# Kernel tuning notes

Measured on AMD Instinct MI355X. Metric: run time of the kernel, lower is better.

Reference implementation:

```python
import jax, jax.numpy as jnp
import numpy as np
import math

N_EMBD = 1024
N_HEAD = 16
B, T = 4, 2048

def setup_inputs() -> dict:
    key = jax.random.key(0)
    k1, k2, k3, k4 = jax.random.split(key, 4)
    x = jax.random.normal(k1, (B, T, N_EMBD), dtype=jnp.float32)
    # torch Linear weights: [out, in]; init scale ~1/sqrt(in)
    s = 1.0 / math.sqrt(N_EMBD)
    W_attn = jax.random.normal(k2, (3 * N_EMBD, N_EMBD), dtype=jnp.float32) * s
    W_proj = jax.random.normal(k3, (N_EMBD, N_EMBD), dtype=jnp.float32) * s
    b_proj = jax.random.normal(k4, (N_EMBD,), dtype=jnp.float32) * s
    return {"x": x, "W_attn": W_attn, "W_proj": W_proj, "b_proj": b_proj}

def reference(x, W_attn, W_proj, b_proj):
    Bx, Tx, C = x.shape
    hd = C // N_HEAD
    qkv = jnp.einsum('btc,oc->bto', x, W_attn)  # [B,T,3C]
    q, k, v = jnp.split(qkv, 3, axis=2)
    # [B, H, T, hd]
    q = q.reshape(Bx, Tx, N_HEAD, hd).transpose(0, 2, 1, 3)
    k = k.reshape(Bx, Tx, N_HEAD, hd).transpose(0, 2, 1, 3)
    v = v.reshape(Bx, Tx, N_HEAD, hd).transpose(0, 2, 1, 3)
    # NOTE: source divides by (1/sqrt(hd)) => MULTIPLIES by sqrt(hd). Faithful.
    att = jnp.einsum('bhqd,bhkd->bhqk', q, k) * jnp.sqrt(jnp.float32(hd))
    causal = jnp.tril(jnp.ones((Tx, Tx), dtype=bool))
    att = jnp.where(causal[None, None, :, :], att, -jnp.inf)
    att = jax.nn.softmax(att, axis=-1)
    y = jnp.einsum('bhqk,bhkd->bhqd', att, v)
    y = y.transpose(0, 2, 1, 3).reshape(Bx, Tx, C)
    y = jnp.einsum('btc,oc->bto', y, W_proj) + b_proj
    return y  # dropout is identity in eval
```

## Files before the change

### kernel.cpp

```cpp
#include <hip/hip_runtime.h>
#include <math.h>

#define BATCH 4
#define TSEQ  2048
#define CEMB  1024
#define NHEAD 16
#define HD    64
#define MROWS (BATCH * TSEQ)
#define QSCALE 11.5415603271f

typedef _Float16 half8 __attribute__((ext_vector_type(8)));
typedef _Float16 half4 __attribute__((ext_vector_type(4)));
typedef float    floatx4 __attribute__((ext_vector_type(4)));

#define GLOBAL_AS __attribute__((address_space(1)))
#define LDS_AS    __attribute__((address_space(3)))

__device__ __forceinline__ void lds_dma16(const _Float16* g, _Float16* l) {
    __builtin_amdgcn_global_load_lds((const GLOBAL_AS unsigned int*)g,
                                     (LDS_AS unsigned int*)l, 16, 0, 0);
}

__device__ __forceinline__ float fast_exp2(float x) {
    float r; asm("v_exp_f32 %0, %1" : "=v"(r) : "v"(x)); return r;
}

__global__ __launch_bounds__(256)
void cvt_fp16(const float* __restrict__ x, const float* __restrict__ wa,
              const float* __restrict__ wp, _Float16* __restrict__ x16,
              _Float16* __restrict__ wa16, _Float16* __restrict__ wp16)
{
    const int n1 = (BATCH * TSEQ * CEMB) / 4;
    const int n2 = (3 * CEMB * CEMB) / 4;
    int i = blockIdx.x * 256 + threadIdx.x;
    const float* src; _Float16* dst; int j;
    if (i < n1)            { src = x;  dst = x16;  j = i; }
    else if (i < n1 + n2)  { src = wa; dst = wa16; j = i - n1; }
    else                   { src = wp; dst = wp16; j = i - n1 - n2; }
    float4 v = ((const float4*)src)[j];
    half4 h = { (_Float16)v.x, (_Float16)v.y, (_Float16)v.z, (_Float16)v.w };
    ((half4*)dst)[j] = h;
}

__device__ __forceinline__ void stage32(const _Float16* __restrict__ gbase,
                                        _Float16* __restrict__ lds,
                                        int row0, int kk, int tid)
{
#pragma unroll
    for (int p = 0; p < 2; ++p) {
        int ci  = p * 256 + tid;
        int row = ci >> 2, pcc = ci & 3;
        int c   = pcc ^ (row & 3);
        lds_dma16(gbase + (size_t)(row0 + row) * CEMB + kk + c * 8, lds + ci * 8);
    }
}

__global__ __launch_bounds__(256)
void qkv_gemm(const _Float16* __restrict__ A, const _Float16* __restrict__ B,
              _Float16* __restrict__ q16, _Float16* __restrict__ k16,
              _Float16* __restrict__ v16)
{
    __shared__ __align__(16) _Float16 smem[16384];
    const int tid = threadIdx.x, lane = tid & 63, wave = tid >> 6;
    const int wm = wave & 1, wn = wave >> 1;
    const int m0 = blockIdx.y * 128, n0 = blockIdx.x * 128;
    const int l15 = lane & 15, quad = lane >> 4;

    floatx4 acc[4][4];
#pragma unroll
    for (int i = 0; i < 4; ++i)
#pragma unroll
        for (int j = 0; j < 4; ++j) acc[i][j] = (floatx4){0.f, 0.f, 0.f, 0.f};

    stage32(A, smem, m0, 0, tid);
    stage32(B, smem + 8192, n0, 0, tid);
    for (int kt = 0; kt < 32; ++kt) {
        const int cur = kt & 1;
        _Float16* Asc = smem + cur * 4096;
        _Float16* Bsc = smem + 8192 + cur * 4096;
        __syncthreads();
        if (kt < 31) {
            stage32(A, smem + (cur ^ 1) * 4096, m0, (kt + 1) * 32, tid);
            stage32(B, smem + 8192 + (cur ^ 1) * 4096, n0, (kt + 1) * 32, tid);
        }
        half8 af[4], bf[4];
#pragma unroll
        for (int mt = 0; mt < 4; ++mt) {
            int row = wm * 64 + mt * 16 + l15;
            af[mt] = *(const half8*)(Asc + row * 32 + (quad ^ (row & 3)) * 8);
        }
#pragma unroll
        for (int nt = 0; nt < 4; ++nt) {
            int row = wn * 64 + nt * 16 + l15;
            bf[nt] = *(const half8*)(Bsc + row * 32 + (quad ^ (row & 3)) * 8);
        }
#pragma unroll
        for (int mt = 0; mt < 4; ++mt)
#pragma unroll
            for (int nt = 0; nt < 4; ++nt)
                acc[mt][nt] = __builtin_amdgcn_mfma_f32_16x16x32_f16(af[mt], bf[nt], acc[mt][nt], 0, 0, 0);
    }

    __syncthreads();
    const int rbase = quad << 2;
    if (n0 < 2 * CEMB) {
        const float scale = (n0 < CEMB) ? QSCALE : 1.0f;
#pragma unroll
        for (int mt = 0; mt < 4; ++mt)
#pragma unroll
            for (int nt = 0; nt < 4; ++nt)
#pragma unroll
                for (int r = 0; r < 4; ++r) {
                    int t = wm * 64 + mt * 16 + rbase + r;
                    int n = wn * 64 + nt * 16 + l15;
                    int pc = (n >> 3) ^ (t & 15);
                    smem[t * 128 + pc * 8 + (n & 7)] = (_Float16)(acc[mt][nt][r] * scale);
                }
        __syncthreads();
        const int chunk = tid & 7;
#pragma unroll
        for (int i = 0; i < 8; ++i) {
            int gr = (tid >> 3) + i * 32;
            int seg = gr >> 7, t = gr & 127;
            int pc = (seg * 8 + chunk) ^ (t & 15);
            half8 v = *(const half8*)(smem + t * 128 + pc * 8);
            int gm = m0 + t, b = gm >> 11, tt = gm & (TSEQ - 1);
            int gnb = n0 + seg * 64;
            _Float16* dst;
            if (n0 < CEMB) {
                int h = gnb >> 6;
                dst = q16 + (((size_t)(b * NHEAD + h)) * TSEQ + tt) * HD;
            } else {
                int h = (gnb - CEMB) >> 6;
                dst = k16 + (((size_t)(b * NHEAD + h)) * TSEQ + tt) * HD;
            }
            *(half8*)(dst + chunk * 8) = v;
        }
    } else {
#pragma unroll
        for (int mt = 0; mt < 4; ++mt)
#pragma unroll
            for (int nt = 0; nt < 4; ++nt)
#pragma unroll
                for (int r = 0; r < 4; ++r) {
                    int t = wm * 64 + mt * 16 + rbase + r;
                    int n = wn * 64 + nt * 16 + l15;
                    int pc = (t >> 3) ^ (n & 15);
                    smem[n * 128 + pc * 8 + (t & 7)] = (_Float16)acc[mt][nt][r];
                }
        __syncthreads();
        const int chunk = tid & 15;
        const int b = m0 >> 11, tblk = m0 & (TSEQ - 1);
#pragma unroll
        for (int i = 0; i < 8; ++i) {
            int row = (tid >> 4) + i * 16;
            int pc = chunk ^ (row & 15);
            half8 v = *(const half8*)(smem + row * 128 + pc * 8);
            int c2 = n0 - 2 * CEMB + row;
            int h = c2 >> 6, d = c2 & 63;
            *(half8*)(v16 + (((size_t)(b * NHEAD + h)) * HD + d) * TSEQ + tblk + chunk * 8) = v;
        }
    }
}

__device__ __forceinline__ void attn_tile(
    const half8& qf0, const half8& qf1,
    float& m_i, float& l_i, floatx4 (&o)[4],
    const _Float16* __restrict__ Ks, const _Float16* __restrict__ Vs,
    bool domask, int l15, int quad, int relq)
{
    floatx4 s[4];
#pragma unroll
    for (int nt = 0; nt < 4; ++nt) {
        int row = nt * 16 + l15;
        int pc0 = quad ^ (row & 7);
        half8 kf0 = *(const half8*)(Ks + row * 64 + pc0 * 8);
        half8 kf1 = *(const half8*)(Ks + row * 64 + (pc0 ^ 4) * 8);
        floatx4 z = (floatx4){0.f, 0.f, 0.f, 0.f};
        z = __builtin_amdgcn_mfma_f32_16x16x32_f16(kf0, qf0, z, 0, 0, 0);
        z = __builtin_amdgcn_mfma_f32_16x16x32_f16(kf1, qf1, z, 0, 0, 0);
        s[nt] = z;
    }
    if (domask) {
#pragma unroll
        for (int nt = 0; nt < 4; ++nt)
#pragma unroll
            for (int r = 0; r < 4; ++r)
                if (nt * 16 + quad * 4 + r > relq) s[nt][r] = -INFINITY;
    }
    float mx = m_i;
#pragma unroll
    for (int nt = 0; nt < 4; ++nt)
        mx = fmaxf(mx, fmaxf(fmaxf(s[nt][0], s[nt][1]), fmaxf(s[nt][2], s[nt][3])));
    mx = fmaxf(mx, __shfl_xor(mx, 16, 64));
    mx = fmaxf(mx, __shfl_xor(mx, 32, 64));
    float alpha = fast_exp2(m_i - mx);
    m_i = mx;
    float rs = 0.f;
    half4 p[4];
#pragma unroll
    for (int nt = 0; nt < 4; ++nt) {
        float p0 = fast_exp2(s[nt][0] - mx), p1 = fast_exp2(s[nt][1] - mx);
        float p2 = fast_exp2(s[nt][2] - mx), p3 = fast_exp2(s[nt][3] - mx);
        rs += (p0 + p1) + (p2 + p3);
        p[nt] = (half4){ (_Float16)p0, (_Float16)p1, (_Float16)p2, (_Float16)p3 };
    }
    rs += __shfl_xor(rs, 16, 64);
    rs += __shfl_xor(rs, 32, 64);
    l_i = l_i * alpha + rs;
#pragma unroll
    for (int mt = 0; mt < 4; ++mt)
#pragma unroll
        for (int r = 0; r < 4; ++r) o[mt][r] *= alpha;
#pragma unroll
    for (int mt = 0; mt < 4; ++mt) {
        int d = mt * 16 + l15;
#pragma unroll
        for (int nt = 0; nt < 4; ++nt) {
            int pc = (2 * nt + (quad >> 1)) ^ (d & 7);
            half4 vf = *(const half4*)(Vs + d * 64 + pc * 8 + (quad & 1) * 4);
            o[mt] = __builtin_amdgcn_mfma_f32_16x16x16f16(vf, p[nt], o[mt], 0, 0, 0);
        }
    }
}

__global__ __launch_bounds__(256)
void attn_fwd(const _Float16* __restrict__ q16, const _Float16* __restrict__ k16,
              const _Float16* __restrict__ v16, _Float16* __restrict__ o16)
{
    __shared__ __align__(16) _Float16 Ks[2][64 * 64];
    __shared__ __align__(16) _Float16 Vs[2][64 * 64];
    const int tid = threadIdx.x, lane = tid & 63, wave = tid >> 6;
    const int l15 = lane & 15, quad = lane >> 4;
    const int qtA = blockIdx.x;
    const int qtB = 31 - qtA;
    const int bh = blockIdx.y, b = bh >> 4, h = bh & 15;
    const int q0A = qtA * 64, q0B = qtB * 64;
    const _Float16* qp = q16 + (size_t)bh * TSEQ * HD;
    const _Float16* kp = k16 + (size_t)bh * TSEQ * HD;
    const _Float16* vp = v16 + (size_t)bh * HD * TSEQ;

    const int relq = wave * 16 + l15;
    half8 qA0 = *(const half8*)(qp + (size_t)(q0A + relq) * HD + quad * 8);
    half8 qA1 = *(const half8*)(qp + (size_t)(q0A + relq) * HD + 32 + quad * 8);
    half8 qB0 = *(const half8*)(qp + (size_t)(q0B + relq) * HD + quad * 8);
    half8 qB1 = *(const half8*)(qp + (size_t)(q0B + relq) * HD + 32 + quad * 8);

    float mA = -INFINITY, lA = 0.f, mB = -INFINITY, lB = 0.f;
    floatx4 oA[4], oB[4];
#pragma unroll
    for (int mt = 0; mt < 4; ++mt) { oA[mt] = (floatx4){0.f,0.f,0.f,0.f}; oB[mt] = (floatx4){0.f,0.f,0.f,0.f}; }

#define STAGE_KV(kt0, buf)                                                     \
    {                                                                          \
        _Float16* kd = Ks[buf];                                                \
        _Float16* vd = Vs[buf];                                                \
        _Pragma("unroll")                                                      \
        for (int p = 0; p < 2; ++p) {                                          \
            int ci = p * 256 + tid;                                            \
            int row = ci >> 3;                                                 \
            int c = (ci & 7) ^ (row & 7);                                      \
            lds_dma16(kp + (size_t)((kt0) + row) * HD + c * 8, kd + ci * 8);   \
            lds_dma16(vp + (size_t)row * TSEQ + (kt0) + c * 8, vd + ci * 8);   \
        }                                                                      \
    }

    STAGE_KV(0, 0);
    for (int kt = 0; kt <= qtB; ++kt) {
        const int cur = kt & 1;
        __syncthreads();
        if (kt < qtB) STAGE_KV((kt + 1) * 64, cur ^ 1);
        attn_tile(qB0, qB1, mB, lB, oB, Ks[cur], Vs[cur], (kt == qtB), l15, quad, relq);
        if (kt <= qtA)
            attn_tile(qA0, qA1, mA, lA, oA, Ks[cur], Vs[cur], (kt == qtA), l15, quad, relq);
    }
#undef STAGE_KV

    const float invA = 1.f / lA, invB = 1.f / lB;
    const size_t baseA = ((size_t)(b * TSEQ + q0A + relq)) * CEMB + h * HD + quad * 4;
    const size_t baseB = ((size_t)(b * TSEQ + q0B + relq)) * CEMB + h * HD + quad * 4;
#pragma unroll
    for (int mt = 0; mt < 4; ++mt) {
        half4 ha = { (_Float16)(oA[mt][0] * invA), (_Float16)(oA[mt][1] * invA),
                     (_Float16)(oA[mt][2] * invA), (_Float16)(oA[mt][3] * invA) };
        half4 hb = { (_Float16)(oB[mt][0] * invB), (_Float16)(oB[mt][1] * invB),
                     (_Float16)(oB[mt][2] * invB), (_Float16)(oB[mt][3] * invB) };
        *(half4*)(o16 + baseA + mt * 16) = ha;
        *(half4*)(o16 + baseB + mt * 16) = hb;
    }
}

__global__ __launch_bounds__(256)
void proj_gemm(const _Float16* __restrict__ A, const _Float16* __restrict__ B,
               const float* __restrict__ bias, float* __restrict__ out)
{
    __shared__ __align__(16) _Float16 As2[2][64 * 32];
    __shared__ __align__(16) _Float16 Bs2[2][128 * 32];
    const int tid = threadIdx.x, lane = tid & 63, wave = tid >> 6;
    const int wm = wave & 1, wn = wave >> 1;
    const int m0 = blockIdx.y * 64, n0 = blockIdx.x * 128;
    const int l15 = lane & 15, quad = lane >> 4;

    floatx4 acc[2][4];
#pragma unroll
    for (int i = 0; i < 2; ++i)
#pragma unroll
        for (int j = 0; j < 4; ++j) acc[i][j] = (floatx4){0.f, 0.f, 0.f, 0.f};

#define STAGE_A(kk, buf)                                                       \
    {                                                                          \
        int row = tid >> 2, c = (tid & 3) ^ (row & 3);                         \
        lds_dma16(A + (size_t)(m0 + row) * CEMB + (kk) + c * 8,                \
                  As2[buf] + tid * 8);                                         \
    }

    STAGE_A(0, 0);
    stage32(B, Bs2[0], n0, 0, tid);
    for (int kt = 0; kt < 32; ++kt) {
        const int cur = kt & 1;
        __syncthreads();
        if (kt < 31) {
            STAGE_A((kt + 1) * 32, cur ^ 1);
            stage32(B, Bs2[cur ^ 1], n0, (kt + 1) * 32, tid);
        }
        half8 af[2], bf[4];
#pragma unroll
        for (int mt = 0; mt < 2; ++mt) {
            int row = wm * 32 + mt * 16 + l15;
            af[mt] = *(const half8*)(As2[cur] + row * 32 + (quad ^ (row & 3)) * 8);
        }
#pragma unroll
        for (int nt = 0; nt < 4; ++nt) {
            int row = wn * 64 + nt * 16 + l15;
            bf[nt] = *(const half8*)(Bs2[cur] + row * 32 + (quad ^ (row & 3)) * 8);
        }
#pragma unroll
        for (int mt = 0; mt < 2; ++mt)
#pragma unroll
            for (int nt = 0; nt < 4; ++nt)
                acc[mt][nt] = __builtin_amdgcn_mfma_f32_16x16x32_f16(af[mt], bf[nt], acc[mt][nt], 0, 0, 0);
    }
#undef STAGE_A

    const int rbase = quad << 2;
#pragma unroll
    for (int mt = 0; mt < 2; ++mt)
#pragma unroll
        for (int nt = 0; nt < 4; ++nt) {
            int gn = n0 + wn * 64 + nt * 16 + l15;
            float bb = bias[gn];
#pragma unroll
            for (int r = 0; r < 4; ++r) {
                int gm = m0 + wm * 32 + mt * 16 + rbase + r;
                out[(size_t)gm * CEMB + gn] = acc[mt][nt][r] + bb;
            }
        }
}

extern "C" void kernel_launch(void* const* d_in, const int* in_sizes, int n_in,
                              void* d_out, int out_size, void* d_ws, size_t ws_size,
                              hipStream_t stream) {
    const float* x     = (const float*)d_in[0];
    const float* Wattn = (const float*)d_in[1];
    const float* Wproj = (const float*)d_in[2];
    const float* bproj = (const float*)d_in[3];
    float* out = (float*)d_out;

    const size_t nx  = (size_t)BATCH * TSEQ * CEMB;
    const size_t nwa = (size_t)3 * CEMB * CEMB;
    const size_t nwp = (size_t)CEMB * CEMB;
    const size_t per = (size_t)BATCH * NHEAD * TSEQ * HD;

    _Float16* x16    = (_Float16*)d_ws;
    _Float16* wa16   = x16 + nx;
    _Float16* wp16   = wa16 + nwa;
    _Float16* q16    = wp16 + nwp;
    _Float16* k16    = q16 + per;
    _Float16* v16    = k16 + per;
    _Float16* attn16 = x16;

    const int nconv = (int)((nx + nwa + nwp) / 4);
    cvt_fp16<<<nconv / 256, 256, 0, stream>>>(x, Wattn, Wproj, x16, wa16, wp16);
    qkv_gemm<<<dim3(3 * CEMB / 128, MROWS / 128), 256, 0, stream>>>(x16, wa16, q16, k16, v16);
    attn_fwd<<<dim3(16, BATCH * NHEAD), 256, 0, stream>>>(q16, k16, v16, attn16);
    proj_gemm<<<dim3(CEMB / 128, MROWS / 64), 256, 0, stream>>>(attn16, wp16, bproj, out);
}
```

Before: 302.1 us.

## Remap QKV GEMM and attention blocks for XCD-local L2 reuse

Both the QKV GEMM and attention kernels now take a flat 1D grid and remap block IDs so that blocks landing on the same XCD (round-robin by bid&7) share weight columns or the same batch-head K/V, aiming for better per-XCD L2 hit rates. The attention kernel also drops the paired causal-balancing scheme (two query tiles per block) in favour of one query tile per block, doubling the block count. This trades the previous load balancing for cache locality. Uneven block lengths are now left to the hardware scheduler, and the long diagonal tiles for a head can end up clustered on one XCD.

```diff
diff --git a/kernel.cpp b/kernel.cpp
--- a/kernel.cpp
+++ b/kernel.cpp
@@ -63,7 +63,11 @@
     __shared__ __align__(16) _Float16 smem[16384];
     const int tid = threadIdx.x, lane = tid & 63, wave = tid >> 6;
     const int wm = wave & 1, wn = wave >> 1;
-    const int m0 = blockIdx.y * 128, n0 = blockIdx.x * 128;
+    const int bid = blockIdx.x;
+    const int xcd = bid & 7, w = bid >> 3;
+    const int bx = xcd * 3 + (w >> 6);
+    const int by = w & 63;
+    const int m0 = by * 128, n0 = bx * 128;
     const int l15 = lane & 15, quad = lane >> 4;
 
     floatx4 acc[4][4];
@@ -232,24 +236,24 @@
     __shared__ __align__(16) _Float16 Vs[2][64 * 64];
     const int tid = threadIdx.x, lane = tid & 63, wave = tid >> 6;
     const int l15 = lane & 15, quad = lane >> 4;
-    const int qtA = blockIdx.x;
-    const int qtB = 31 - qtA;
-    const int bh = blockIdx.y, b = bh >> 4, h = bh & 15;
-    const int q0A = qtA * 64, q0B = qtB * 64;
+    const int bid = blockIdx.x;
+    const int xcd = bid & 7, w = bid >> 3;
+    const int bh = xcd * 8 + (w >> 5);
+    const int qt = w & 31;
+    const int b = bh >> 4, h = bh & 15;
+    const int q0 = qt * 64;
     const _Float16* qp = q16 + (size_t)bh * TSEQ * HD;
     const _Float16* kp = k16 + (size_t)bh * TSEQ * HD;
     const _Float16* vp = v16 + (size_t)bh * HD * TSEQ;
 
     const int relq = wave * 16 + l15;
-    half8 qA0 = *(const half8*)(qp + (size_t)(q0A + relq) * HD + quad * 8);
-    half8 qA1 = *(const half8*)(qp + (size_t)(q0A + relq) * HD + 32 + quad * 8);
-    half8 qB0 = *(const half8*)(qp + (size_t)(q0B + relq) * HD + quad * 8);
-    half8 qB1 = *(const half8*)(qp + (size_t)(q0B + relq) * HD + 32 + quad * 8);
-
-    float mA = -INFINITY, lA = 0.f, mB = -INFINITY, lB = 0.f;
-    floatx4 oA[4], oB[4];
-#pragma unroll
-    for (int mt = 0; mt < 4; ++mt) { oA[mt] = (floatx4){0.f,0.f,0.f,0.f}; oB[mt] = (floatx4){0.f,0.f,0.f,0.f}; }
+    half8 q0f = *(const half8*)(qp + (size_t)(q0 + relq) * HD + quad * 8);
+    half8 q1f = *(const half8*)(qp + (size_t)(q0 + relq) * HD + 32 + quad * 8);
+
+    float m_i = -INFINITY, l_i = 0.f;
+    floatx4 o[4];
+#pragma unroll
+    for (int mt = 0; mt < 4; ++mt) o[mt] = (floatx4){0.f,0.f,0.f,0.f};
 
 #define STAGE_KV(kt0, buf)                                                     \
     {                                                                          \
@@ -266,27 +270,21 @@
     }
 
     STAGE_KV(0, 0);
-    for (int kt = 0; kt <= qtB; ++kt) {
+    for (int kt = 0; kt <= qt; ++kt) {
         const int cur = kt & 1;
         __syncthreads();
-        if (kt < qtB) STAGE_KV((kt + 1) * 64, cur ^ 1);
-        attn_tile(qB0, qB1, mB, lB, oB, Ks[cur], Vs[cur], (kt == qtB), l15, quad, relq);
-        if (kt <= qtA)
-            attn_tile(qA0, qA1, mA, lA, oA, Ks[cur], Vs[cur], (kt == qtA), l15, quad, relq);
+        if (kt < qt) STAGE_KV((kt + 1) * 64, cur ^ 1);
+        attn_tile(q0f, q1f, m_i, l_i, o, Ks[cur], Vs[cur], (kt == qt), l15, quad, relq);
     }
 #undef STAGE_KV
 
-    const float invA = 1.f / lA, invB = 1.f / lB;
-    const size_t baseA = ((size_t)(b * TSEQ + q0A + relq)) * CEMB + h * HD + quad * 4;
-    const size_t baseB = ((size_t)(b * TSEQ + q0B + relq)) * CEMB + h * HD + quad * 4;
+    const float inv = 1.f / l_i;
+    const size_t base = ((size_t)(b * TSEQ + q0 + relq)) * CEMB + h * HD + quad * 4;
 #pragma unroll
     for (int mt = 0; mt < 4; ++mt) {
-        half4 ha = { (_Float16)(oA[mt][0] * invA), (_Float16)(oA[mt][1] * invA),
-                     (_Float16)(oA[mt][2] * invA), (_Float16)(oA[mt][3] * invA) };
-        half4 hb = { (_Float16)(oB[mt][0] * invB), (_Float16)(oB[mt][1] * invB),
-                     (_Float16)(oB[mt][2] * invB), (_Float16)(oB[mt][3] * invB) };
-        *(half4*)(o16 + baseA + mt * 16) = ha;
-        *(half4*)(o16 + baseB + mt * 16) = hb;
+        half4 hv = { (_Float16)(o[mt][0] * inv), (_Float16)(o[mt][1] * inv),
+                     (_Float16)(o[mt][2] * inv), (_Float16)(o[mt][3] * inv) };
+        *(half4*)(o16 + base + mt * 16) = hv;
     }
 }
 
@@ -381,7 +379,7 @@
 
     const int nconv = (int)((nx + nwa + nwp) / 4);
     cvt_fp16<<<nconv / 256, 256, 0, stream>>>(x, Wattn, Wproj, x16, wa16, wp16);
-    qkv_gemm<<<dim3(3 * CEMB / 128, MROWS / 128), 256, 0, stream>>>(x16, wa16, q16, k16, v16);
-    attn_fwd<<<dim3(16, BATCH * NHEAD), 256, 0, stream>>>(q16, k16, v16, attn16);
+    qkv_gemm<<<1536, 256, 0, stream>>>(x16, wa16, q16, k16, v16);
+    attn_fwd<<<2048, 256, 0, stream>>>(q16, k16, v16, attn16);
     proj_gemm<<<dim3(CEMB / 128, MROWS / 64), 256, 0, stream>>>(attn16, wp16, bproj, out);
 }
```

New measurement: 304.6 us. No clear change (+0.8%).
